# Optimization experiments

Hardware: AMD Instinct MI355X
Metric: run time of the kernel (lower is better)

The kernel has to match this reference:

```python
import jax, jax.numpy as jnp
import numpy as np

N = 50000      # nodes
E = 800000     # edges (before self-loops)
IN = 128       # in_channels
C = 64         # hidden_channels
HD = 4         # heads
SLOPE = 0.2    # GATConv leaky_relu negative slope
EPS_BN = 1e-5


def add_self_loops(edge_index, n):
    loop = jnp.arange(n, dtype=edge_index.dtype)
    return jnp.concatenate([edge_index, jnp.stack([loop, loop])], axis=1)


def gat_conv(x, edge_index, W, a_src, a_dst, bias, heads, out_c, concat, n):
    src, dst = edge_index[0], edge_index[1]
    h = (x @ W).reshape(n, heads, out_c)                 # [N,H,C]
    al_s = jnp.sum(h * a_src, axis=-1)                   # [N,H]
    al_d = jnp.sum(h * a_dst, axis=-1)                   # [N,H]
    e = jax.nn.leaky_relu(al_s[src] + al_d[dst], SLOPE)  # [Etot,H]
    m = jax.ops.segment_max(e, dst, num_segments=n)      # segment softmax (stable)
    ex = jnp.exp(e - m[dst])
    s = jax.ops.segment_sum(ex, dst, num_segments=n)
    alpha = ex / (s[dst] + 1e-16)                        # [Etot,H]
    out = jax.ops.segment_sum(h[src] * alpha[:, :, None], dst, num_segments=n)
    out = out.reshape(n, heads * out_c) if concat else out.mean(axis=1)
    return out + bias


def batch_norm(x, gamma, beta):
    mu = x.mean(axis=0)
    var = x.var(axis=0)
    return (x - mu) * jax.lax.rsqrt(var + EPS_BN) * gamma + beta


def setup_inputs() -> dict:
    key = jax.random.key(0)
    ks = jax.random.split(key, 24)
    f = lambda k, shp, sc: (jax.random.normal(k, shp, dtype=jnp.float32) * sc)
    HC = HD * C
    return {
        "x": f(ks[0], (N, IN), 1.0),
        "edge_index": jax.random.randint(ks[1], (2, E), 0, N, dtype=jnp.int64),
        # conv1: IN -> C, heads=HD, concat
        "W1": f(ks[2], (IN, HC), 0.05), "as1": f(ks[3], (HD, C), 0.05),
        "ad1": f(ks[4], (HD, C), 0.05), "b1": f(ks[5], (HC,), 0.02),
        "g1": jnp.ones((HC,), jnp.float32), "bb1": jnp.zeros((HC,), jnp.float32),
        # conv2: HC -> C, heads=HD, concat
        "W2": f(ks[6], (HC, HC), 0.05), "as2": f(ks[7], (HD, C), 0.05),
        "ad2": f(ks[8], (HD, C), 0.05), "b2": f(ks[9], (HC,), 0.02),
        "g2": jnp.ones((HC,), jnp.float32), "bb2": jnp.zeros((HC,), jnp.float32),
        # conv3: HC -> C, heads=1, mean
        "W3": f(ks[10], (HC, C), 0.05), "as3": f(ks[11], (1, C), 0.05),
        "ad3": f(ks[12], (1, C), 0.05), "b3": f(ks[13], (C,), 0.02),
        # skips
        "Ws1": f(ks[14], (IN, HC), 0.05), "bs1": f(ks[15], (HC,), 0.02),
        "Ws2": f(ks[16], (HC, C), 0.05), "bs2": f(ks[17], (C,), 0.02),
    }


def reference(x, edge_index, W1, as1, ad1, b1, g1, bb1,
              W2, as2, ad2, b2, g2, bb2,
              W3, as3, ad3, b3, Ws1, bs1, Ws2, bs2):
    ei = add_self_loops(edge_index, N)
    x_init = x @ Ws1 + bs1
    h = gat_conv(x, ei, W1, as1, ad1, b1, HD, C, True, N)
    h = jax.nn.elu(batch_norm(h, g1, bb1)) + x_init
    x_skip = h @ Ws2 + bs2
    h = gat_conv(h, ei, W2, as2, ad2, b2, HD, C, True, N)
    h = jax.nn.elu(batch_norm(h, g2, bb2))
    out = gat_conv(h, ei, W3, as3, ad3, b3, 1, C, False, N) + x_skip
    return out
```

## Files before the change

### kernel.cpp

```cpp
#include <hip/hip_runtime.h>
#include <hip/hip_bf16.h>
#include <cstdint>
#include <cstddef>


#define LRELU_SLOPE 0.2f

typedef __attribute__((ext_vector_type(8))) short short8;
typedef __attribute__((ext_vector_type(4))) float f32x4;

__device__ __forceinline__ float bf2f(unsigned short u) {
  union { unsigned int i; float f; } t; t.i = ((unsigned int)u) << 16; return t.f;
}
__device__ __forceinline__ unsigned short f2bf(float f) {
  __hip_bfloat16 h = __float2bfloat16(f);
  return *reinterpret_cast<unsigned short*>(&h);
}

template<int K, int WAVES_GAT, int WAVES_SKIP>
__global__ __launch_bounds__((WAVES_GAT + WAVES_SKIP) * 64)
void gemm_gat_fused(const unsigned short* __restrict__ A,
                    const unsigned short* __restrict__ BtH,
                    const unsigned short* __restrict__ BtS,
                    const float* __restrict__ a_s, const float* __restrict__ a_d,
                    const float* __restrict__ biasS,
                    unsigned short* __restrict__ Hout,
                    float* __restrict__ als, float* __restrict__ ald,
                    unsigned short* __restrict__ Sout, int M) {
  constexpr int NKS = K / 32;
  constexpr int NH  = WAVES_GAT * 64;
  constexpr int NS  = WAVES_SKIP * 64;
  const int wid  = threadIdx.x >> 6;
  const int lane = threadIdx.x & 63;
  const int r    = lane & 15;
  const int q    = lane >> 4;
  const int koff = q * 8;
  const bool isGat = wid < WAVES_GAT;
  const int colbase = isGat ? wid * 64 : (wid - WAVES_GAT) * 64;
  const unsigned short* Bt = isGat ? BtH : BtS;

  short8 b[4][NKS];
  #pragma unroll
  for (int nf = 0; nf < 4; ++nf)
    #pragma unroll
    for (int ks = 0; ks < NKS; ++ks)
      b[nf][ks] = *(const short8*)(Bt + (size_t)(colbase + nf * 16 + r) * K + ks * 32 + koff);

  float as4[4] = {}, ad4[4] = {};
  if (isGat) {
    #pragma unroll
    for (int nf = 0; nf < 4; ++nf) {
      as4[nf] = a_s[colbase + nf * 16 + r];
      ad4[nf] = a_d[colbase + nf * 16 + r];
    }
  }

  const int ntiles = (M + 15) >> 4;
  const int chunk = (ntiles + 7) >> 3;
  const int xcd   = blockIdx.x & 7;
  const int lo    = xcd * chunk;
  const int hi    = min(lo + chunk, ntiles);
  const int bstep = gridDim.x >> 3;
  for (int t = lo + (blockIdx.x >> 3); t < hi; t += bstep) {
    const int row = t * 16 + r;
    short8 a[NKS];
    #pragma unroll
    for (int ks = 0; ks < NKS; ++ks) {
      a[ks] = (short8)(short)0;
      if (row < M) a[ks] = *(const short8*)(A + (size_t)row * K + ks * 32 + koff);
    }
    f32x4 acc[4];
    #pragma unroll
    for (int nf = 0; nf < 4; ++nf) acc[nf] = (f32x4)0.0f;
    #pragma unroll
    for (int ks = 0; ks < NKS; ++ks)
      #pragma unroll
      for (int nf = 0; nf < 4; ++nf)
        acc[nf] = __builtin_amdgcn_mfma_f32_16x16x32_bf16(a[ks], b[nf][ks], acc[nf], 0, 0, 0);

    const int rbase = t * 16 + q * 4;
    if (isGat) {
      #pragma unroll
      for (int nf = 0; nf < 4; ++nf) {
        const int col = colbase + nf * 16 + r;
        #pragma unroll
        for (int i = 0; i < 4; ++i) {
          const int rr = rbase + i;
          if (rr < M) Hout[(size_t)rr * NH + col] = f2bf(acc[nf][i]);
        }
      }
      #pragma unroll
      for (int i = 0; i < 4; ++i) {
        float s = 0.f, d = 0.f;
        #pragma unroll
        for (int nf = 0; nf < 4; ++nf) {
          s = fmaf(acc[nf][i], as4[nf], s);
          d = fmaf(acc[nf][i], ad4[nf], d);
        }
        #pragma unroll
        for (int m = 8; m >= 1; m >>= 1) {
          s += __shfl_xor(s, m, 64);
          d += __shfl_xor(d, m, 64);
        }
        const int rr = rbase + i;
        if (r == 0 && rr < M) {
          als[(size_t)rr * WAVES_GAT + wid] = s;
          ald[(size_t)rr * WAVES_GAT + wid] = d;
        }
      }
    } else {
      #pragma unroll
      for (int nf = 0; nf < 4; ++nf) {
        const int col = colbase + nf * 16 + r;
        const float bs = biasS[col];
        #pragma unroll
        for (int i = 0; i < 4; ++i) {
          const int rr = rbase + i;
          if (rr < M) Sout[(size_t)rr * NS + col] = f2bf(acc[nf][i] + bs);
        }
      }
    }
  }
}

__global__ __launch_bounds__(256)
void gemm_gat3(const unsigned short* __restrict__ A, const unsigned short* __restrict__ Bt,
               const float* __restrict__ a_s, const float* __restrict__ a_d,
               unsigned short* __restrict__ Hout, float* __restrict__ als,
               float* __restrict__ ald, int M) {
  constexpr int K = 256, NKS = 8;
  const int wid  = threadIdx.x >> 6;
  const int lane = threadIdx.x & 63;
  const int r    = lane & 15;
  const int q    = lane >> 4;
  const int koff = q * 8;

  short8 b[4][NKS];
  #pragma unroll
  for (int nf = 0; nf < 4; ++nf)
    #pragma unroll
    for (int ks = 0; ks < NKS; ++ks)
      b[nf][ks] = *(const short8*)(Bt + (size_t)(nf * 16 + r) * K + ks * 32 + koff);
  float as4[4], ad4[4];
  #pragma unroll
  for (int nf = 0; nf < 4; ++nf) {
    as4[nf] = a_s[nf * 16 + r];
    ad4[nf] = a_d[nf * 16 + r];
  }

  const int ntiles = (M + 15) >> 4;
  const int chunk = (ntiles + 7) >> 3;
  const int xcd   = blockIdx.x & 7;
  const int lo    = xcd * chunk;
  const int hi    = min(lo + chunk, ntiles);
  const int bstep = (gridDim.x >> 3) * 4;
  for (int t = lo + (blockIdx.x >> 3) * 4 + wid; t < hi; t += bstep) {
    const int row = t * 16 + r;
    short8 a[NKS];
    #pragma unroll
    for (int ks = 0; ks < NKS; ++ks) {
      a[ks] = (short8)(short)0;
      if (row < M) a[ks] = *(const short8*)(A + (size_t)row * K + ks * 32 + koff);
    }
    f32x4 acc[4];
    #pragma unroll
    for (int nf = 0; nf < 4; ++nf) acc[nf] = (f32x4)0.0f;
    #pragma unroll
    for (int ks = 0; ks < NKS; ++ks)
      #pragma unroll
      for (int nf = 0; nf < 4; ++nf)
        acc[nf] = __builtin_amdgcn_mfma_f32_16x16x32_bf16(a[ks], b[nf][ks], acc[nf], 0, 0, 0);

    const int rbase = t * 16 + q * 4;
    #pragma unroll
    for (int nf = 0; nf < 4; ++nf) {
      const int col = nf * 16 + r;
      #pragma unroll
      for (int i = 0; i < 4; ++i) {
        const int rr = rbase + i;
        if (rr < M) Hout[(size_t)rr * 64 + col] = f2bf(acc[nf][i]);
      }
    }
    #pragma unroll
    for (int i = 0; i < 4; ++i) {
      float s = 0.f, d = 0.f;
      #pragma unroll
      for (int nf = 0; nf < 4; ++nf) {
        s = fmaf(acc[nf][i], as4[nf], s);
        d = fmaf(acc[nf][i], ad4[nf], d);
      }
      #pragma unroll
      for (int m = 8; m >= 1; m >>= 1) {
        s += __shfl_xor(s, m, 64);
        d += __shfl_xor(d, m, 64);
      }
      const int rr = rbase + i;
      if (r == 0 && rr < M) { als[rr] = s; ald[rr] = d; }
    }
  }
}

__global__ __launch_bounds__(256)
void prep_all(const float* __restrict__ x,
              const float* __restrict__ W1, const float* __restrict__ Ws1,
              const float* __restrict__ W2, const float* __restrict__ Ws2,
              const float* __restrict__ W3,
              unsigned short* __restrict__ xb,
              unsigned short* __restrict__ W1t, unsigned short* __restrict__ Ws1t,
              unsigned short* __restrict__ W2t, unsigned short* __restrict__ Ws2t,
              unsigned short* __restrict__ W3t, float* __restrict__ sums, int n) {
  int idx = blockIdx.x * blockDim.x + threadIdx.x;
  const int nx = n * 32;
  if (idx < nx) {
    float4 v = ((const float4*)x)[idx];
    ushort4 o;
    o.x = f2bf(v.x); o.y = f2bf(v.y); o.z = f2bf(v.z); o.w = f2bf(v.w);
    ((ushort4*)xb)[idx] = o;
    return;
  }
  idx -= nx;
  if (idx < 256 * 128) { int nn = idx >> 7, kk = idx & 127; W1t[idx]  = f2bf(W1[kk * 256 + nn]);  return; }
  idx -= 256 * 128;
  if (idx < 256 * 128) { int nn = idx >> 7, kk = idx & 127; Ws1t[idx] = f2bf(Ws1[kk * 256 + nn]); return; }
  idx -= 256 * 128;
  if (idx < 256 * 256) { int nn = idx >> 8, kk = idx & 255; W2t[idx]  = f2bf(W2[kk * 256 + nn]);  return; }
  idx -= 256 * 256;
  if (idx < 64 * 256)  { int nn = idx >> 8, kk = idx & 255; Ws2t[idx] = f2bf(Ws2[kk * 64 + nn]);  return; }
  idx -= 64 * 256;
  if (idx < 64 * 256)  { int nn = idx >> 8, kk = idx & 255; W3t[idx]  = f2bf(W3[kk * 64 + nn]); return; }
  idx -= 64 * 256;
  if (idx < 512) sums[idx] = 0.f;
}

__global__ void count_edges(const int* __restrict__ ei, int E, int* __restrict__ counts,
                            int n) {
  const int g = blockIdx.x & 7;
  const int chunk = (n + 7) >> 3;
  const int lo = g * chunk, hi = min(lo + chunk, n);
  const int stride = (gridDim.x >> 3) * blockDim.x;
  for (int i = (blockIdx.x >> 3) * blockDim.x + threadIdx.x; i < E; i += stride) {
    int d = ei[E + i];
    if (d >= lo && d < hi) atomicAdd(&counts[d], 1);
  }
}
__global__ void scan_block(const int* __restrict__ in, int* __restrict__ out,
                           int* __restrict__ bsums, int n) {
  __shared__ int tmp[256];
  int t = threadIdx.x;
  int gid = blockIdx.x * 256 + t;
  int v = (gid < n) ? in[gid] : 0;
  tmp[t] = v;
  __syncthreads();
  #pragma unroll
  for (int off = 1; off < 256; off <<= 1) {
    int x = (t >= off) ? tmp[t - off] : 0;
    __syncthreads();
    tmp[t] += x;
    __syncthreads();
  }
  if (gid < n) out[gid] = tmp[t] - v;
  if (t == 255) bsums[blockIdx.x] = tmp[255];
}
__global__ void scan_tops(const int* __restrict__ bsums, int* __restrict__ boffs, int nb) {
  __shared__ int tmp[256];
  int t = threadIdx.x;
  int v = (t < nb) ? bsums[t] : 0;
  tmp[t] = v;
  __syncthreads();
  #pragma unroll
  for (int off = 1; off < 256; off <<= 1) {
    int x = (t >= off) ? tmp[t - off] : 0;
    __syncthreads();
    tmp[t] += x;
    __syncthreads();
  }
  if (t < nb) boffs[t] = tmp[t] - v;
}
__global__ void scan_add(int* __restrict__ rp, const int* __restrict__ boffs,
                         int n, int etot) {
  int gid = blockIdx.x * 256 + threadIdx.x;
  if (gid < n) rp[gid] += boffs[blockIdx.x];
  if (gid == 0) rp[n] = etot;
}
__global__ void fill_edges(const int* __restrict__ ei, int E, const int* __restrict__ rp,
                           int* __restrict__ cursor, int* __restrict__ csr, int n) {
  const int g = blockIdx.x & 7;
  const int chunk = (n + 7) >> 3;
  const int lo = g * chunk, hi = min(lo + chunk, n);
  const int stride = (gridDim.x >> 3) * blockDim.x;
  for (int i = (blockIdx.x >> 3) * blockDim.x + threadIdx.x; i < E; i += stride) {
    int d = ei[E + i];
    if (d >= lo && d < hi) {
      int pos = rp[d] + atomicAdd(&cursor[d], 1);
      csr[pos] = ei[i];
    }
  }
}

template<int HEADS, int HCt, bool OUT_BF16, bool STATS>
__global__ __launch_bounds__(256)
void gat_aggregate(const unsigned short* __restrict__ H, const float* __restrict__ als,
                   const float* __restrict__ ald, const int* __restrict__ rp,
                   const int* __restrict__ csr, const float* __restrict__ bias,
                   const unsigned short* __restrict__ skip, void* __restrict__ out,
                   float* __restrict__ sums, int n) {
  constexpr int CPL = HCt / 64;
  const int wid  = threadIdx.x >> 6;
  const int lane = threadIdx.x & 63;
  const int myhead = (HEADS == 1) ? 0 : (lane >> 4);
  const int gw0 = blockIdx.x * 4 + wid;
  const int nw  = gridDim.x * 4;
  float ls[CPL] = {}, lq[CPL] = {};

  for (int w = gw0; w < n; w += nw) {
    const int beg = rp[w], end = rp[w + 1];
    const float adh = ald[(size_t)w * HEADS + myhead];

    auto att = [&](int s) -> float {
      float e = als[(size_t)s * HEADS + myhead] + adh;
      e = fmaxf(e, LRELU_SLOPE * e);
      return __expf(e);
    };

    float acc[CPL];
    float ssum = att(w);
    {
      const unsigned short* hp = H + (size_t)w * HCt + lane * CPL;
      if constexpr (CPL == 4) {
        ushort4 hv = *(const ushort4*)hp;
        acc[0] = ssum * bf2f(hv.x); acc[1] = ssum * bf2f(hv.y);
        acc[2] = ssum * bf2f(hv.z); acc[3] = ssum * bf2f(hv.w);
      } else {
        acc[0] = ssum * bf2f(hp[0]);
      }
    }

    int j = beg;
    for (; j + 8 <= end; j += 8) {
      int sidx[8];
      #pragma unroll
      for (int u = 0; u < 8; ++u) sidx[u] = csr[j + u];
      const int myS = csr[j + (lane & 7)];
      float e = als[(size_t)myS * HEADS + myhead] + adh;
      e = fmaxf(e, LRELU_SLOPE * e);
      e = __expf(e);
      float ex[8];
      #pragma unroll
      for (int u = 0; u < 8; ++u) ex[u] = __shfl(e, (lane & 48) | u, 64);
      if constexpr (CPL == 4) {
        ushort4 hv[8];
        #pragma unroll
        for (int u = 0; u < 8; ++u)
          hv[u] = *(const ushort4*)(H + (size_t)sidx[u] * HCt + lane * 4);
        #pragma unroll
        for (int u = 0; u < 8; ++u) {
          ssum += ex[u];
          acc[0] = fmaf(ex[u], bf2f(hv[u].x), acc[0]);
          acc[1] = fmaf(ex[u], bf2f(hv[u].y), acc[1]);
          acc[2] = fmaf(ex[u], bf2f(hv[u].z), acc[2]);
          acc[3] = fmaf(ex[u], bf2f(hv[u].w), acc[3]);
        }
      } else {
        unsigned short hv[8];
        #pragma unroll
        for (int u = 0; u < 8; ++u) hv[u] = H[(size_t)sidx[u] * HCt + lane];
        #pragma unroll
        for (int u = 0; u < 8; ++u) {
          ssum += ex[u];
          acc[0] = fmaf(ex[u], bf2f(hv[u]), acc[0]);
        }
      }
    }
    for (; j + 4 <= end; j += 4) {
      int sidx[4];
      #pragma unroll
      for (int u = 0; u < 4; ++u) sidx[u] = csr[j + u];
      float ex[4];
      #pragma unroll
      for (int u = 0; u < 4; ++u) ex[u] = att(sidx[u]);
      if constexpr (CPL == 4) {
        ushort4 hv[4];
        #pragma unroll
        for (int u = 0; u < 4; ++u)
          hv[u] = *(const ushort4*)(H + (size_t)sidx[u] * HCt + lane * 4);
        #pragma unroll
        for (int u = 0; u < 4; ++u) {
          ssum += ex[u];
          acc[0] = fmaf(ex[u], bf2f(hv[u].x), acc[0]);
          acc[1] = fmaf(ex[u], bf2f(hv[u].y), acc[1]);
          acc[2] = fmaf(ex[u], bf2f(hv[u].z), acc[2]);
          acc[3] = fmaf(ex[u], bf2f(hv[u].w), acc[3]);
        }
      } else {
        unsigned short hv[4];
        #pragma unroll
        for (int u = 0; u < 4; ++u) hv[u] = H[(size_t)sidx[u] * HCt + lane];
        #pragma unroll
        for (int u = 0; u < 4; ++u) {
          ssum += ex[u];
          acc[0] = fmaf(ex[u], bf2f(hv[u]), acc[0]);
        }
      }
    }
    for (; j < end; ++j) {
      const int s = csr[j];
      const float ex = att(s);
      ssum += ex;
      const unsigned short* hp = H + (size_t)s * HCt + lane * CPL;
      if constexpr (CPL == 4) {
        ushort4 hv = *(const ushort4*)hp;
        acc[0] = fmaf(ex, bf2f(hv.x), acc[0]);
        acc[1] = fmaf(ex, bf2f(hv.y), acc[1]);
        acc[2] = fmaf(ex, bf2f(hv.z), acc[2]);
        acc[3] = fmaf(ex, bf2f(hv.w), acc[3]);
      } else {
        acc[0] = fmaf(ex, bf2f(hp[0]), acc[0]);
      }
    }

    const float inv = 1.f / (ssum + 1e-16f);
    #pragma unroll
    for (int c = 0; c < CPL; ++c) {
      int ch = lane * CPL + c;
      float v = acc[c] * inv + bias[ch];
      if (skip) v += bf2f(skip[(size_t)w * HCt + ch]);
      if constexpr (STATS) {
        ls[c] += v;
        lq[c] = fmaf(v, v, lq[c]);
      }
      if constexpr (OUT_BF16)
        ((unsigned short*)out)[(size_t)w * HCt + ch] = f2bf(v);
      else
        ((float*)out)[(size_t)w * HCt + ch] = v;
    }
  }

  if constexpr (STATS) {
    __shared__ float red[512];
    if (threadIdx.x < 256) { red[threadIdx.x] = 0.f; red[256 + threadIdx.x] = 0.f; }
    __syncthreads();
    #pragma unroll
    for (int c = 0; c < CPL; ++c) {
      atomicAdd(&red[lane * CPL + c], ls[c]);
      atomicAdd(&red[256 + lane * CPL + c], lq[c]);
    }
    __syncthreads();
    if (threadIdx.x < 256) {
      atomicAdd(&sums[threadIdx.x], red[threadIdx.x]);
      atomicAdd(&sums[256 + threadIdx.x], red[256 + threadIdx.x]);
    }
  }
}

__global__ void bn_finalize(float* __restrict__ sums, const float* __restrict__ gamma,
                            const float* __restrict__ beta, float* __restrict__ scsh,
                            int n) {
  int c = threadIdx.x;
  if (c < 256) {
    float mean = sums[c] / (float)n;
    float var = sums[256 + c] / (float)n - mean * mean;
    float sc = gamma[c] * rsqrtf(var + 1e-5f);
    scsh[c] = sc;
    scsh[256 + c] = beta[c] - mean * sc;
    sums[c] = 0.f;
    sums[256 + c] = 0.f;
  }
}
__global__ __launch_bounds__(256)
void bn_apply_elu(const unsigned short* __restrict__ X, const float* __restrict__ scsh,
                  const unsigned short* __restrict__ skip, unsigned short* __restrict__ Y,
                  int total) {
  int i4 = blockIdx.x * blockDim.x + threadIdx.x;
  if (i4 * 4 >= total) return;
  ushort4 xv = ((const ushort4*)X)[i4];
  int cb = (i4 * 4) & 255;
  float4 sc = *(const float4*)(scsh + cb);
  float4 sh = *(const float4*)(scsh + 256 + cb);
  float4 y;
  y.x = fmaf(bf2f(xv.x), sc.x, sh.x);
  y.y = fmaf(bf2f(xv.y), sc.y, sh.y);
  y.z = fmaf(bf2f(xv.z), sc.z, sh.z);
  y.w = fmaf(bf2f(xv.w), sc.w, sh.w);
  y.x = (y.x > 0.f) ? y.x : expm1f(y.x);
  y.y = (y.y > 0.f) ? y.y : expm1f(y.y);
  y.z = (y.z > 0.f) ? y.z : expm1f(y.z);
  y.w = (y.w > 0.f) ? y.w : expm1f(y.w);
  if (skip) {
    ushort4 s4 = ((const ushort4*)skip)[i4];
    y.x += bf2f(s4.x); y.y += bf2f(s4.y); y.z += bf2f(s4.z); y.w += bf2f(s4.w);
  }
  ushort4 o;
  o.x = f2bf(y.x); o.y = f2bf(y.y); o.z = f2bf(y.z); o.w = f2bf(y.w);
  ((ushort4*)Y)[i4] = o;
}

extern "C" void kernel_launch(void* const* d_in, const int* in_sizes, int n_in,
                              void* d_out, int out_size, void* d_ws, size_t ws_size,
                              hipStream_t stream) {
  const float* x   = (const float*)d_in[0];
  const int*   ei  = (const int*)d_in[1];
  const float* W1  = (const float*)d_in[2];
  const float* as1 = (const float*)d_in[3];
  const float* ad1 = (const float*)d_in[4];
  const float* b1  = (const float*)d_in[5];
  const float* g1  = (const float*)d_in[6];
  const float* bb1 = (const float*)d_in[7];
  const float* W2  = (const float*)d_in[8];
  const float* as2 = (const float*)d_in[9];
  const float* ad2 = (const float*)d_in[10];
  const float* b2  = (const float*)d_in[11];
  const float* g2  = (const float*)d_in[12];
  const float* bb2 = (const float*)d_in[13];
  const float* W3  = (const float*)d_in[14];
  const float* as3 = (const float*)d_in[15];
  const float* ad3 = (const float*)d_in[16];
  const float* b3  = (const float*)d_in[17];
  const float* Ws1 = (const float*)d_in[18];
  const float* bs1 = (const float*)d_in[19];
  const float* Ws2 = (const float*)d_in[20];
  const float* bs2 = (const float*)d_in[21];

  const int n = in_sizes[0] / 128;
  const int E = in_sizes[1] / 2;

  char* wsp = (char*)d_ws;
  auto carve = [&](size_t bytes) -> void* {
    void* p = (void*)wsp;
    wsp += (bytes + 255) & ~(size_t)255;
    return p;
  };
  unsigned short* Hb  = (unsigned short*)carve((size_t)n * 256 * 2);
  unsigned short* hb  = (unsigned short*)carve((size_t)n * 256 * 2);
  unsigned short* xbD = (unsigned short*)carve((size_t)n * 128 * 2);
  unsigned short* xb  = xbD;
  unsigned short* D   = xbD;
  unsigned short* Bv  = (unsigned short*)carve((size_t)n * 256 * 2);
  unsigned short* Cv  = (unsigned short*)carve((size_t)n * 256 * 2);
  float* als  = (float*)carve((size_t)n * 4 * 4);
  float* ald  = (float*)carve((size_t)n * 4 * 4);
  int*   rp   = (int*)carve((size_t)(n + 1) * 4);
  int*   cnt  = (int*)carve((size_t)n * 4);
  int*   bsums= (int*)carve(256 * 4);
  int*   boffs= (int*)carve(256 * 4);
  int*   csr  = (int*)carve((size_t)E * 4);
  float* bnb  = (float*)carve(4 * 256 * 4);
  float* sums = bnb;
  float* scsh = bnb + 512;
  unsigned short* W1t  = (unsigned short*)carve(128 * 256 * 2);
  unsigned short* Ws1t = (unsigned short*)carve(128 * 256 * 2);
  unsigned short* W2t  = (unsigned short*)carve(256 * 256 * 2);
  unsigned short* Ws2t = (unsigned short*)carve(256 * 64 * 2);
  unsigned short* W3t  = (unsigned short*)carve(256 * 64 * 2);

  const int NB = (n + 255) / 256;

  hipMemsetAsync(cnt, 0, (size_t)n * 4, stream);
  count_edges<<<2048, 256, 0, stream>>>(ei, E, cnt, n);
  scan_block<<<NB, 256, 0, stream>>>(cnt, rp, bsums, n);
  scan_tops<<<1, 256, 0, stream>>>(bsums, boffs, NB);
  scan_add<<<NB, 256, 0, stream>>>(rp, boffs, n, E);
  hipMemsetAsync(cnt, 0, (size_t)n * 4, stream);
  fill_edges<<<2048, 256, 0, stream>>>(ei, E, rp, cnt, csr, n);

  {
    const int total = n * 32 + 2 * 256 * 128 + 256 * 256 + 2 * 64 * 256 + 512;
    prep_all<<<(total + 255) / 256, 256, 0, stream>>>(x, W1, Ws1, W2, Ws2, W3,
                                                      xb, W1t, Ws1t, W2t, Ws2t, W3t,
                                                      sums, n);
  }

  const int agrid = 2048;
  const int egrid = (n * 256 / 4 + 255) / 256;

  gemm_gat_fused<128, 4, 4><<<512, 512, 0, stream>>>(
      xb, W1t, Ws1t, as1, ad1, bs1, Hb, als, ald, Bv, n);
  gat_aggregate<4, 256, true, true><<<agrid, 256, 0, stream>>>(
      Hb, als, ald, rp, csr, b1, nullptr, Cv, sums, n);
  bn_finalize<<<1, 256, 0, stream>>>(sums, g1, bb1, scsh, n);
  bn_apply_elu<<<egrid, 256, 0, stream>>>(Cv, scsh, Bv, hb, n * 256);

  gemm_gat_fused<256, 4, 1><<<512, 320, 0, stream>>>(
      hb, W2t, Ws2t, as2, ad2, bs2, Hb, als, ald, D, n);
  gat_aggregate<4, 256, true, true><<<agrid, 256, 0, stream>>>(
      Hb, als, ald, rp, csr, b2, nullptr, Cv, sums, n);
  bn_finalize<<<1, 256, 0, stream>>>(sums, g2, bb2, scsh, n);
  bn_apply_elu<<<egrid, 256, 0, stream>>>(Cv, scsh, nullptr, hb, n * 256);

  gemm_gat3<<<512, 256, 0, stream>>>(hb, W3t, as3, ad3, Hb, als, ald, n);
  gat_aggregate<1, 64, false, false><<<agrid, 256, 0, stream>>>(
      Hb, als, ald, rp, csr, b3, D, d_out, nullptr, n);
}
```

Baseline: 489.7 us.

## Launch one wave per node in GAT aggregation with replicated BN stat buffers

The aggregation kernel drops its grid-stride loop over nodes and launches one wavefront per destination node, so the grid grows from 2048 blocks to about n/4 blocks. The 8-edge inner loop now computes attention per edge directly instead of computing once per lane group and broadcasting with shuffles. To handle the larger number of blocks doing global atomics for batch-norm statistics, the sums buffer is replicated 8 ways by block index, and bn_finalize reduces and clears the replicas. The aim is better load balance across nodes of uneven degree and more latency hiding, at the cost of more blocks and more per-block shared-memory reduction and atomic traffic.

```diff
diff --git a/kernel.cpp b/kernel.cpp
--- a/kernel.cpp
+++ b/kernel.cpp
@@ -229,7 +229,7 @@
   idx -= 64 * 256;
   if (idx < 64 * 256)  { int nn = idx >> 8, kk = idx & 255; W3t[idx]  = f2bf(W3[kk * 64 + nn]); return; }
   idx -= 64 * 256;
-  if (idx < 512) sums[idx] = 0.f;
+  if (idx < 8 * 512) sums[idx] = 0.f;
 }
 
 __global__ void count_edges(const int* __restrict__ ei, int E, int* __restrict__ counts,
@@ -305,15 +305,13 @@
                    const unsigned short* __restrict__ skip, void* __restrict__ out,
                    float* __restrict__ sums, int n) {
   constexpr int CPL = HCt / 64;
-  const int wid  = threadIdx.x >> 6;
+  const int w = (blockIdx.x * blockDim.x + threadIdx.x) >> 6;
   const int lane = threadIdx.x & 63;
-  const int myhead = (HEADS == 1) ? 0 : (lane >> 4);
-  const int gw0 = blockIdx.x * 4 + wid;
-  const int nw  = gridDim.x * 4;
   float ls[CPL] = {}, lq[CPL] = {};
 
-  for (int w = gw0; w < n; w += nw) {
+  if (w < n) {
     const int beg = rp[w], end = rp[w + 1];
+    const int myhead = (HEADS == 1) ? 0 : (lane >> 4);
     const float adh = ald[(size_t)w * HEADS + myhead];
 
     auto att = [&](int s) -> float {
@@ -340,18 +338,14 @@
       int sidx[8];
       #pragma unroll
       for (int u = 0; u < 8; ++u) sidx[u] = csr[j + u];
-      const int myS = csr[j + (lane & 7)];
-      float e = als[(size_t)myS * HEADS + myhead] + adh;
-      e = fmaxf(e, LRELU_SLOPE * e);
-      e = __expf(e);
-      float ex[8];
-      #pragma unroll
-      for (int u = 0; u < 8; ++u) ex[u] = __shfl(e, (lane & 48) | u, 64);
       if constexpr (CPL == 4) {
         ushort4 hv[8];
         #pragma unroll
         for (int u = 0; u < 8; ++u)
           hv[u] = *(const ushort4*)(H + (size_t)sidx[u] * HCt + lane * 4);
+        float ex[8];
+        #pragma unroll
+        for (int u = 0; u < 8; ++u) ex[u] = att(sidx[u]);
         #pragma unroll
         for (int u = 0; u < 8; ++u) {
           ssum += ex[u];
@@ -364,6 +358,9 @@
         unsigned short hv[8];
         #pragma unroll
         for (int u = 0; u < 8; ++u) hv[u] = H[(size_t)sidx[u] * HCt + lane];
+        float ex[8];
+        #pragma unroll
+        for (int u = 0; u < 8; ++u) ex[u] = att(sidx[u]);
         #pragma unroll
         for (int u = 0; u < 8; ++u) {
           ssum += ex[u];
@@ -425,8 +422,8 @@
       float v = acc[c] * inv + bias[ch];
       if (skip) v += bf2f(skip[(size_t)w * HCt + ch]);
       if constexpr (STATS) {
-        ls[c] += v;
-        lq[c] = fmaf(v, v, lq[c]);
+        ls[c] = v;
+        lq[c] = v * v;
       }
       if constexpr (OUT_BF16)
         ((unsigned short*)out)[(size_t)w * HCt + ch] = f2bf(v);
@@ -439,15 +436,18 @@
     __shared__ float red[512];
     if (threadIdx.x < 256) { red[threadIdx.x] = 0.f; red[256 + threadIdx.x] = 0.f; }
     __syncthreads();
-    #pragma unroll
-    for (int c = 0; c < CPL; ++c) {
-      atomicAdd(&red[lane * CPL + c], ls[c]);
-      atomicAdd(&red[256 + lane * CPL + c], lq[c]);
+    if (w < n) {
+      #pragma unroll
+      for (int c = 0; c < CPL; ++c) {
+        atomicAdd(&red[lane * CPL + c], ls[c]);
+        atomicAdd(&red[256 + lane * CPL + c], lq[c]);
+      }
     }
     __syncthreads();
+    float* srep = sums + (size_t)(blockIdx.x & 7) * 512;
     if (threadIdx.x < 256) {
-      atomicAdd(&sums[threadIdx.x], red[threadIdx.x]);
-      atomicAdd(&sums[256 + threadIdx.x], red[256 + threadIdx.x]);
+      atomicAdd(&srep[threadIdx.x], red[threadIdx.x]);
+      atomicAdd(&srep[256 + threadIdx.x], red[256 + threadIdx.x]);
     }
   }
 }
@@ -457,13 +457,19 @@
                             int n) {
   int c = threadIdx.x;
   if (c < 256) {
-    float mean = sums[c] / (float)n;
-    float var = sums[256 + c] / (float)n - mean * mean;
+    float s = 0.f, q = 0.f;
+    #pragma unroll
+    for (int r = 0; r < 8; ++r) {
+      s += sums[r * 512 + c];
+      q += sums[r * 512 + 256 + c];
+      sums[r * 512 + c] = 0.f;
+      sums[r * 512 + 256 + c] = 0.f;
+    }
+    float mean = s / (float)n;
+    float var = q / (float)n - mean * mean;
     float sc = gamma[c] * rsqrtf(var + 1e-5f);
     scsh[c] = sc;
     scsh[256 + c] = beta[c] - mean * sc;
-    sums[c] = 0.f;
-    sums[256 + c] = 0.f;
   }
 }
 __global__ __launch_bounds__(256)
@@ -543,9 +549,9 @@
   int*   bsums= (int*)carve(256 * 4);
   int*   boffs= (int*)carve(256 * 4);
   int*   csr  = (int*)carve((size_t)E * 4);
-  float* bnb  = (float*)carve(4 * 256 * 4);
+  float* bnb  = (float*)carve((8 * 512 + 512) * 4);
   float* sums = bnb;
-  float* scsh = bnb + 512;
+  float* scsh = bnb + 8 * 512;
   unsigned short* W1t  = (unsigned short*)carve(128 * 256 * 2);
   unsigned short* Ws1t = (unsigned short*)carve(128 * 256 * 2);
   unsigned short* W2t  = (unsigned short*)carve(256 * 256 * 2);
@@ -563,30 +569,30 @@
   fill_edges<<<2048, 256, 0, stream>>>(ei, E, rp, cnt, csr, n);
 
   {
-    const int total = n * 32 + 2 * 256 * 128 + 256 * 256 + 2 * 64 * 256 + 512;
+    const int total = n * 32 + 2 * 256 * 128 + 256 * 256 + 2 * 64 * 256 + 8 * 512;
     prep_all<<<(total + 255) / 256, 256, 0, stream>>>(x, W1, Ws1, W2, Ws2, W3,
                                                       xb, W1t, Ws1t, W2t, Ws2t, W3t,
                                                       sums, n);
   }
 
-  const int agrid = 2048;
+  const int wgrid = (n * 64 + 255) / 256;
   const int egrid = (n * 256 / 4 + 255) / 256;
 
   gemm_gat_fused<128, 4, 4><<<512, 512, 0, stream>>>(
       xb, W1t, Ws1t, as1, ad1, bs1, Hb, als, ald, Bv, n);
-  gat_aggregate<4, 256, true, true><<<agrid, 256, 0, stream>>>(
+  gat_aggregate<4, 256, true, true><<<wgrid, 256, 0, stream>>>(
       Hb, als, ald, rp, csr, b1, nullptr, Cv, sums, n);
   bn_finalize<<<1, 256, 0, stream>>>(sums, g1, bb1, scsh, n);
   bn_apply_elu<<<egrid, 256, 0, stream>>>(Cv, scsh, Bv, hb, n * 256);
 
   gemm_gat_fused<256, 4, 1><<<512, 320, 0, stream>>>(
       hb, W2t, Ws2t, as2, ad2, bs2, Hb, als, ald, D, n);
-  gat_aggregate<4, 256, true, true><<<agrid, 256, 0, stream>>>(
+  gat_aggregate<4, 256, true, true><<<wgrid, 256, 0, stream>>>(
       Hb, als, ald, rp, csr, b2, nullptr, Cv, sums, n);
   bn_finalize<<<1, 256, 0, stream>>>(sums, g2, bb2, scsh, n);
   bn_apply_elu<<<egrid, 256, 0, stream>>>(Cv, scsh, nullptr, hb, n * 256);
 
   gemm_gat3<<<512, 256, 0, stream>>>(hb, W3t, as3, ad3, Hb, als, ald, n);
-  gat_aggregate<1, 64, false, false><<<agrid, 256, 0, stream>>>(
+  gat_aggregate<1, 64, false, false><<<wgrid, 256, 0, stream>>>(
       Hb, als, ald, rp, csr, b3, D, d_out, nullptr, n);
 }
```

Result: slower. 553.2 us (+13.0%).
